# Performance work log

Measured on AMD Instinct MI355X. Metric: run time of the kernel, lower is better.

Reference implementation:

```python
import jax, jax.numpy as jnp
import numpy as np

B = 4096
FEATURES = 4608 + 4608 + 8 + 1  # 9225
LSTM = 512
R = FEATURES / LSTM
D1 = int(FEATURES / R ** (1.0 / 3.0))
D2 = int(FEATURES / R ** (2.0 / 3.0))
ACTION_SHAPES = (64, 64, 64, 64, 64, 64, 64, 64)


def setup_inputs() -> dict:
    key = jax.random.key(0)
    ks = jax.random.split(key, 32)
    s = 0.02
    inp = {
        "actualCanvasFeatures": jax.random.normal(ks[0], (B, 4608), jnp.float32),
        "objectiveCanvasFeatures": jax.random.normal(ks[1], (B, 4608), jnp.float32),
        "last_action": jax.random.uniform(ks[2], (B, 8), jnp.float32),
        "episode_percentage": 0,
        # encoder MLP
        "W1": jax.random.normal(ks[3], (FEATURES, D1), jnp.float32) * s,
        "b1": jnp.zeros((D1,), jnp.float32),
        "W2": jax.random.normal(ks[4], (D1, D2), jnp.float32) * s,
        "b2": jnp.zeros((D2,), jnp.float32),
        "W3": jax.random.normal(ks[5], (D2, LSTM), jnp.float32) * s,
        "b3": jnp.zeros((LSTM,), jnp.float32),
        # LSTM (torch gate order i,f,g,o)
        "Wih": jax.random.normal(ks[6], (4 * LSTM, LSTM), jnp.float32) * s,
        "Whh": jax.random.normal(ks[7], (4 * LSTM, LSTM), jnp.float32) * s,
        "bih": jnp.zeros((4 * LSTM,), jnp.float32),
        "bhh": jnp.zeros((4 * LSTM,), jnp.float32),
        "h0": jnp.zeros((B, LSTM), jnp.float32),
        "c0": jnp.zeros((B, LSTM), jnp.float32),
        # decoder
        "dW1": jax.random.normal(ks[8], (LSTM, LSTM // 2), jnp.float32) * s,
        "db1": jnp.zeros((LSTM // 2,), jnp.float32),
        "headWs": tuple(jax.random.normal(ks[9 + i], (LSTM // 2, a), jnp.float32) * s
                        for i, a in enumerate(ACTION_SHAPES)),
        "headbs": tuple(jnp.zeros((a,), jnp.float32) for a in ACTION_SHAPES),
        "dWo": jax.random.normal(ks[20], (LSTM + 1, LSTM), jnp.float32) * s,
        "dbo": jnp.zeros((LSTM,), jnp.float32),
    }
    return inp


def reference(actualCanvasFeatures, objectiveCanvasFeatures, last_action,
              episode_percentage, W1, b1, W2, b2, W3, b3, Wih, Whh, bih, bhh,
              h0, c0, dW1, db1, headWs, headbs, dWo, dbo):
    b = actualCanvasFeatures.shape[0]
    ep = jnp.full((b, 1), episode_percentage, dtype=jnp.float32)
    feats = jnp.concatenate(
        [actualCanvasFeatures, objectiveCanvasFeatures, last_action, ep], axis=1)
    # encoder MLP (dropout is eval-mode identity)
    x = jax.nn.relu(feats @ W1 + b1)
    x = jax.nn.relu(x @ W2 + b2)
    x = jax.nn.relu(x @ W3 + b3)
    # single-step LSTM cell, torch gate order i,f,g,o
    gates = x @ Wih.T + bih + h0 @ Whh.T + bhh
    i, f, g, o = jnp.split(gates, 4, axis=1)
    c = jax.nn.sigmoid(f) * c0 + jax.nn.sigmoid(i) * jnp.tanh(g)
    z = jax.nn.sigmoid(o) * jnp.tanh(c)  # seed
    key = jax.random.key(42)
    actions = []
    log_probabilities = jnp.zeros((b,), jnp.float32)
    entropy = jnp.float32(0.0)
    for Wk, bk in zip(headWs, headbs):
        z1 = jax.nn.relu(z @ dW1 + db1)
        logits = z1 @ Wk + bk
        logp = jax.nn.log_softmax(logits, axis=1)
        probs = jnp.exp(logp)
        key, sk = jax.random.split(key)
        act = jax.random.categorical(sk, logits, axis=1)  # [b] int
        actions.append(act.astype(jnp.float32))
        entropy = entropy + jnp.sum(-jnp.sum(probs * logp, axis=1))
        log_probabilities = log_probabilities + jnp.take_along_axis(
            logp, act[:, None], axis=1)[:, 0]
        z = jax.nn.relu(
            jnp.concatenate([z, act.astype(jnp.float32)[:, None]], axis=1) @ dWo + dbo)
    action = jnp.stack(actions, axis=1)  # [b, n_sub_actions]
    return action, entropy, log_probabilities
```

## Files before the change

kernel.cpp:

```cpp
#include <hip/hip_runtime.h>
#include <cstdint>
#include <cstring>

typedef _Float16 f16;
typedef _Float16 f16x8 __attribute__((ext_vector_type(8)));
typedef float f32x4 __attribute__((ext_vector_type(4)));

static constexpr int kPartitionable = 1;

struct Ptr8 { const float* p[8]; };

__device__ __host__ __forceinline__ int swz(int r, int k) {
  return k ^ ((r & 7) << 3);
}

__device__ __forceinline__ void gload16(const void* g, void* l) {
  __builtin_amdgcn_global_load_lds(
      (const __attribute__((address_space(1))) unsigned int*)g,
      (__attribute__((address_space(3))) unsigned int*)l, 16, 0, 0);
}

__host__ __device__ inline void tf2x32(uint32_t k0, uint32_t k1,
                                       uint32_t x0, uint32_t x1,
                                       uint32_t& o0, uint32_t& o1) {
  uint32_t ks[3] = {k0, k1, k0 ^ k1 ^ 0x1BD11BDAu};
  uint32_t v0 = x0 + ks[0], v1 = x1 + ks[1];
  const int r0[4] = {13, 15, 26, 6};
  const int r1[4] = {17, 29, 16, 24};
  for (int g = 0; g < 5; ++g) {
    const int* rr = (g & 1) ? r1 : r0;
    for (int j = 0; j < 4; ++j) {
      v0 += v1;
      v1 = (v1 << rr[j]) | (v1 >> (32 - rr[j]));
      v1 ^= v0;
    }
    v0 += ks[(g + 1) % 3];
    v1 += ks[(g + 2) % 3] + (uint32_t)(g + 1);
  }
  o0 = v0; o1 = v1;
}

template <int BM, int BN>
__global__ __launch_bounds__(256, 2) void gemm_split(
    const f16* __restrict__ Ah, const f16* __restrict__ Al, int lda,
    const f16* __restrict__ Bh, const f16* __restrict__ Bl, int ldb,
    int K,
    const float* __restrict__ bias1, const float* __restrict__ bias2,
    int nReal, int relu, int writeF32,
    float* __restrict__ outF, f16* __restrict__ outH, f16* __restrict__ outL,
    int ldo) {
  constexpr int BK = 64;
  constexpr int TM = BM / 32;
  constexpr int TN = BN / 32;
  static_assert(BM == BN, "square tiles only");
  __shared__ f16 sAh[BM * BK];
  __shared__ f16 sAl[BM * BK];
  __shared__ f16 sBh[BN * BK];
  __shared__ f16 sBl[BN * BK];

  const int tid = threadIdx.x;
  const int wave = tid >> 6;
  const int lane = tid & 63;
  const int wm = wave & 1, wn = wave >> 1;
  const int m0 = blockIdx.x * BM;
  const int n0 = blockIdx.y * BN;

  f32x4 acc[TM][TN];
  const f32x4 zero = {0.f, 0.f, 0.f, 0.f};
#pragma unroll
  for (int i = 0; i < TM; ++i)
#pragma unroll
    for (int j = 0; j < TN; ++j) acc[i][j] = zero;

  const f16* src;
  f16* dst;
  int ld, base;
  if (wave == 0)      { src = Ah; dst = sAh; ld = lda; base = m0; }
  else if (wave == 1) { src = Al; dst = sAl; ld = lda; base = m0; }
  else if (wave == 2) { src = Bh; dst = sBh; ld = ldb; base = n0; }
  else                { src = Bl; dst = sBl; ld = ldb; base = n0; }
  constexpr int NITER = BM / 8;
  const f16* gbase = src + (size_t)(base + (lane >> 3)) * ld + (lane & 7) * 8;

  const int fr = lane & 15;
  const int q8 = (lane >> 4) * 8;
  const int sw = (fr & 7) << 3;

  for (int k0 = 0; k0 < K; k0 += BK) {
    __syncthreads();
#pragma unroll
    for (int j = 0; j < NITER; ++j)
      gload16(gbase + (size_t)(j * 8) * ld + k0, dst + j * 512);
    __syncthreads();
#pragma unroll
    for (int kk = 0; kk < BK; kk += 32) {
      const int kf = (kk + q8) ^ sw;
      f16x8 aH[TM], aL[TM], bH[TN], bL[TN];
#pragma unroll
      for (int i = 0; i < TM; ++i) {
        int off = (wm * (BM / 2) + i * 16 + fr) * BK + kf;
        aH[i] = *(const f16x8*)&sAh[off];
        aL[i] = *(const f16x8*)&sAl[off];
      }
#pragma unroll
      for (int j = 0; j < TN; ++j) {
        int off = (wn * (BN / 2) + j * 16 + fr) * BK + kf;
        bH[j] = *(const f16x8*)&sBh[off];
        bL[j] = *(const f16x8*)&sBl[off];
      }
#pragma unroll
      for (int i = 0; i < TM; ++i)
#pragma unroll
        for (int j = 0; j < TN; ++j) {
          acc[i][j] = __builtin_amdgcn_mfma_f32_16x16x32_f16(aH[i], bH[j], acc[i][j], 0, 0, 0);
          acc[i][j] = __builtin_amdgcn_mfma_f32_16x16x32_f16(aH[i], bL[j], acc[i][j], 0, 0, 0);
          acc[i][j] = __builtin_amdgcn_mfma_f32_16x16x32_f16(aL[i], bH[j], acc[i][j], 0, 0, 0);
        }
    }
  }
  const int rq = lane >> 4, cl = lane & 15;
#pragma unroll
  for (int i = 0; i < TM; ++i)
#pragma unroll
    for (int j = 0; j < TN; ++j)
#pragma unroll
      for (int r = 0; r < 4; ++r) {
        int row = m0 + wm * (BM / 2) + i * 16 + rq * 4 + r;
        int col = n0 + wn * (BN / 2) + j * 16 + cl;
        float v = acc[i][j][r];
        if (col < nReal) {
          if (bias1) v += bias1[col];
          if (bias2) v += bias2[col];
          if (relu) v = fmaxf(v, 0.f);
        } else {
          v = 0.f;
        }
        if (writeF32) {
          outF[(size_t)row * ldo + col] = v;
        } else {
          size_t o = (size_t)row * ldo + swz(row, col);
          f16 h = (f16)v;
          outH[o] = h;
          outL[o] = (f16)(v - (float)h);
        }
      }
}

__global__ void conv_feats(const float* __restrict__ A, const float* __restrict__ O,
                           const float* __restrict__ LA, const int* __restrict__ EP,
                           f16* __restrict__ H, f16* __restrict__ L) {
  uint32_t idx = blockIdx.x * 256u + threadIdx.x;
  const uint32_t total = 4096u * 9280u;
  if (idx >= total) return;
  uint32_t b = idx / 9280u, c = idx - b * 9280u;
  float v;
  if (c < 4608u) v = A[(size_t)b * 4608 + c];
  else if (c < 9216u) v = O[(size_t)b * 4608 + (c - 4608u)];
  else if (c < 9224u) v = LA[(size_t)b * 8 + (c - 9216u)];
  else if (c == 9224u) v = (float)EP[0];
  else v = 0.f;
  size_t o = (size_t)b * 9280 + swz((int)b, (int)c);
  f16 h = (f16)v;
  H[o] = h;
  L[o] = (f16)(v - (float)h);
}

__global__ void convT_kernel(const float* __restrict__ W, int Kreal, int Nreal,
                             f16* __restrict__ BtH, f16* __restrict__ BtL, int Kpad) {
  __shared__ float tile[32][33];
  int k0 = blockIdx.x * 32, n0 = blockIdx.y * 32;
  int tx = threadIdx.x, ty = threadIdx.y;
  for (int r = 0; r < 32; r += 8) {
    int k = k0 + ty + r, n = n0 + tx;
    float v = (k < Kreal && n < Nreal) ? W[(size_t)k * Nreal + n] : 0.f;
    tile[ty + r][tx] = v;
  }
  __syncthreads();
  for (int r = 0; r < 32; r += 8) {
    int n = n0 + ty + r, k = k0 + tx;
    float v = tile[tx][ty + r];
    size_t o = (size_t)n * Kpad + swz(n, k);
    f16 h = (f16)v;
    BtH[o] = h;
    BtL[o] = (f16)(v - (float)h);
  }
}

__global__ void convT_heads(Ptr8 ws, f16* __restrict__ BtH, f16* __restrict__ BtL) {
  __shared__ float tile[32][33];
  int h = blockIdx.z;
  const float* W = ws.p[h];
  int k0 = blockIdx.x * 32, n0 = blockIdx.y * 32;
  int tx = threadIdx.x, ty = threadIdx.y;
  for (int r = 0; r < 32; r += 8) {
    int k = k0 + ty + r, n = n0 + tx;
    float v = (k < 256 && n < 64) ? W[(size_t)k * 64 + n] : 0.f;
    tile[ty + r][tx] = v;
  }
  __syncthreads();
  size_t base = (size_t)h * 64 * 256;
  for (int r = 0; r < 32; r += 8) {
    int n = n0 + ty + r, k = k0 + tx;
    float v = tile[tx][ty + r];
    size_t o = base + (size_t)n * 256 + swz(n, k);
    f16 hh = (f16)v;
    BtH[o] = hh;
    BtL[o] = (f16)(v - (float)hh);
  }
}

__global__ void conv_lstmB(const float* __restrict__ Wih, const float* __restrict__ Whh,
                           f16* __restrict__ H, f16* __restrict__ L) {
  uint32_t idx = blockIdx.x * 256u + threadIdx.x;
  uint32_t n = idx >> 10, k = idx & 1023u;
  float v = (k < 512u) ? Wih[(size_t)n * 512 + k] : Whh[(size_t)n * 512 + (k - 512u)];
  size_t o = (size_t)n * 1024 + swz((int)n, (int)k);
  f16 h = (f16)v;
  H[o] = h;
  L[o] = (f16)(v - (float)h);
}

__global__ void conv_h0(const float* __restrict__ h0, f16* __restrict__ H, f16* __restrict__ L) {
  uint32_t idx = blockIdx.x * 256u + threadIdx.x;
  uint32_t b = idx >> 9, j = idx & 511u;
  float v = h0[idx];
  size_t o = (size_t)b * 1024 + swz((int)b, (int)(512 + j));
  f16 h = (f16)v;
  H[o] = h;
  L[o] = (f16)(v - (float)h);
}

__global__ void lstm_pointwise(const float* __restrict__ gates, const float* __restrict__ c0,
                               f16* __restrict__ zH, f16* __restrict__ zL) {
  uint32_t idx = blockIdx.x * 256u + threadIdx.x;
  uint32_t b = idx >> 9, n = idx & 511u;
  const float* g = gates + (size_t)b * 2048;
  float gi = g[n], gf = g[512 + n], gg = g[1024 + n], go = g[1536 + n];
  float si = 1.f / (1.f + expf(-gi));
  float sf = 1.f / (1.f + expf(-gf));
  float so = 1.f / (1.f + expf(-go));
  float c = sf * c0[idx] + si * tanhf(gg);
  float z = so * tanhf(c);
  size_t o = (size_t)b * 576 + swz((int)b, (int)n);
  f16 h = (f16)z;
  zH[o] = h;
  zL[o] = (f16)(z - (float)h);
}

__global__ void init_ws(f16* zAH, f16* zAL, f16* zBH, f16* zBL,
                        float* wsLogp, float* wsEnt) {
  uint32_t idx = blockIdx.x * 256u + threadIdx.x;
  if (idx < 4096u * 63u) {
    uint32_t b = idx / 63u, c = 513u + idx - b * 63u;
    size_t o = (size_t)b * 576 + swz((int)b, (int)c);
    zAH[o] = (f16)0.f; zAL[o] = (f16)0.f; zBH[o] = (f16)0.f; zBL[o] = (f16)0.f;
  }
  if (idx < 4096u) wsLogp[idx] = 0.f;
  if (idx == 0) *wsEnt = 0.f;
}

__device__ inline double shfl_xor_dbl(double v, int m) {
  union { double d; int i[2]; } u;
  u.d = v;
  u.i[0] = __shfl_xor(u.i[0], m);
  u.i[1] = __shfl_xor(u.i[1], m);
  return u.d;
}

__global__ void sample_head(const float* __restrict__ logits,
                            uint32_t sk0, uint32_t sk1, int head, int partitionable,
                            float* __restrict__ outAct,
                            f16* __restrict__ zH, f16* __restrict__ zL,
                            float* __restrict__ wsLogp, float* __restrict__ wsEnt) {
  int wave = threadIdx.x >> 6, lane = threadIdx.x & 63;
  int b = blockIdx.x * 4 + wave;
  float l = logits[(size_t)b * 64 + lane];

  uint32_t i = (uint32_t)b * 64u + (uint32_t)lane;
  uint32_t bits;
  if (partitionable) {
    uint32_t o0, o1;
    tf2x32(sk0, sk1, 0u, i, o0, o1);
    bits = o0 ^ o1;
  } else {
    const uint32_t H = 131072u;
    uint32_t c0, c1, o0, o1;
    int pick;
    if (i < H) { c0 = i; c1 = i + H; pick = 0; }
    else       { c0 = i - H; c1 = i; pick = 1; }
    tf2x32(sk0, sk1, c0, c1, o0, o1);
    bits = pick ? o1 : o0;
  }
  uint32_t ub = (bits >> 9) | 0x3f800000u;
  float u;
  __builtin_memcpy(&u, &ub, 4);
  u -= 1.0f;
  if (u == 0.0f) u = 1.17549435e-38f;
  double gum = -log(-log((double)u));
  double s = (double)l + gum;

  int bi = lane;
  double bv = s;
#pragma unroll
  for (int off = 1; off < 64; off <<= 1) {
    double ov = shfl_xor_dbl(bv, off);
    int oi = __shfl_xor(bi, off);
    if (ov > bv || (ov == bv && oi < bi)) { bv = ov; bi = oi; }
  }
  int act = bi;

  float m = l;
#pragma unroll
  for (int off = 1; off < 64; off <<= 1) m = fmaxf(m, __shfl_xor(m, off));
  float e = expf(l - m);
  float S = e, D = e * l;
#pragma unroll
  for (int off = 1; off < 64; off <<= 1) {
    S += __shfl_xor(S, off);
    D += __shfl_xor(D, off);
  }
  float M = m + logf(S);
  float Hrow = M - D / S;
  float l_act = __shfl(l, act);

  if (lane == 0) {
    outAct[(size_t)b * 8 + head] = (float)act;
    wsLogp[b] += (l_act - M);
    size_t zo = (size_t)b * 576 + swz(b, 512);
    zH[zo] = (f16)act;
    zL[zo] = (f16)0.f;
  }
  __shared__ float hs[4];
  if (lane == 0) hs[wave] = Hrow;
  __syncthreads();
  if (threadIdx.x == 0) atomicAdd(wsEnt, hs[0] + hs[1] + hs[2] + hs[3]);
}

__global__ void finalize_out(const float* __restrict__ wsEnt, const float* __restrict__ wsLogp,
                             float* __restrict__ out) {
  uint32_t idx = blockIdx.x * 256u + threadIdx.x;
  if (idx == 0) out[32768] = *wsEnt;
  if (idx < 4096u) out[32769 + idx] = wsLogp[idx];
}

extern "C" void kernel_launch(void* const* d_in, const int* in_sizes, int n_in,
                              void* d_out, int out_size, void* d_ws, size_t ws_size,
                              hipStream_t stream) {
  (void)in_sizes; (void)out_size; (void)ws_size;
  const float* actual = (const float*)d_in[0];
  const float* object = (const float*)d_in[1];
  const float* lastA = (const float*)d_in[2];
  const int* ep = (const int*)d_in[3];
  const float* W1 = (const float*)d_in[4];
  const float* b1 = (const float*)d_in[5];
  const float* W2 = (const float*)d_in[6];
  const float* b2 = (const float*)d_in[7];
  const float* W3 = (const float*)d_in[8];
  const float* b3 = (const float*)d_in[9];
  const float* Wih = (const float*)d_in[10];
  const float* Whh = (const float*)d_in[11];
  const float* bih = (const float*)d_in[12];
  const float* bhh = (const float*)d_in[13];
  const float* h0 = (const float*)d_in[14];
  const float* c0 = (const float*)d_in[15];
  const float* dW1 = (const float*)d_in[16];
  const float* db1 = (const float*)d_in[17];
  const float* headW[8];
  const float* headb[8];
  const float *dWo, *dbo;
  if (n_in >= 36) {
    for (int h = 0; h < 8; ++h) headW[h] = (const float*)d_in[18 + h];
    for (int h = 0; h < 8; ++h) headb[h] = (const float*)d_in[26 + h];
    dWo = (const float*)d_in[34];
    dbo = (const float*)d_in[35];
  } else {
    const float* hw = (const float*)d_in[18];
    const float* hbp = (const float*)d_in[19];
    for (int h = 0; h < 8; ++h) { headW[h] = hw + (size_t)h * 256 * 64; headb[h] = hbp + (size_t)h * 64; }
    dWo = (const float*)d_in[20];
    dbo = (const float*)d_in[21];
  }

  constexpr int Bq = 4096;
  constexpr int K1 = 9280, N1 = 3584, N1r = 3518;
  constexpr int K2 = 3584, N2 = 1408, N2r = 1342;
  constexpr int K3 = 1408, N3 = 512;
  constexpr int KL = 1024, NL = 2048;
  constexpr int KD1 = 512, ND1 = 256;
  constexpr int KH = 256;
  constexpr int KDO = 576, NDO = 512;

  uint8_t* w = (uint8_t*)d_ws;
  size_t off = 0;
  auto alloc = [&](size_t bytes) -> void* {
    off = (off + 1023) & ~(size_t)1023;
    void* p = w + off;
    off += bytes;
    return p;
  };
  f16* A1h = (f16*)alloc((size_t)Bq * K1 * 2);
  f16* A1l = (f16*)alloc((size_t)Bq * K1 * 2);
  f16* Bt1h = (f16*)alloc((size_t)N1 * K1 * 2);
  f16* Bt1l = (f16*)alloc((size_t)N1 * K1 * 2);
  f16* x1h = (f16*)alloc((size_t)Bq * K2 * 2);
  f16* x1l = (f16*)alloc((size_t)Bq * K2 * 2);
  f16* Bt2h = (f16*)alloc((size_t)N2 * K2 * 2);
  f16* Bt2l = (f16*)alloc((size_t)N2 * K2 * 2);
  size_t poff = 0;
  auto palloc = [&](size_t bytes) -> void* {
    poff = (poff + 1023) & ~(size_t)1023;
    void* p = w + poff;
    poff += bytes;
    return p;
  };
  f16* x2h = (f16*)palloc((size_t)Bq * K3 * 2);
  f16* x2l = (f16*)palloc((size_t)Bq * K3 * 2);
  f16* Bt3h = (f16*)palloc((size_t)N3 * K3 * 2);
  f16* Bt3l = (f16*)palloc((size_t)N3 * K3 * 2);
  f16* ALh = (f16*)palloc((size_t)Bq * KL * 2);
  f16* ALl = (f16*)palloc((size_t)Bq * KL * 2);
  f16* BLh = (f16*)palloc((size_t)NL * KL * 2);
  f16* BLl = (f16*)palloc((size_t)NL * KL * 2);
  float* gates = (float*)palloc((size_t)Bq * NL * 4);
  f16* zAH = (f16*)palloc((size_t)Bq * 576 * 2);
  f16* zAL = (f16*)palloc((size_t)Bq * 576 * 2);
  f16* zBH = (f16*)palloc((size_t)Bq * 576 * 2);
  f16* zBL = (f16*)palloc((size_t)Bq * 576 * 2);
  f16* Btd1h = (f16*)palloc((size_t)ND1 * KD1 * 2);
  f16* Btd1l = (f16*)palloc((size_t)ND1 * KD1 * 2);
  f16* z1h = (f16*)palloc((size_t)Bq * ND1 * 2);
  f16* z1l = (f16*)palloc((size_t)Bq * ND1 * 2);
  f16* Bthh = (f16*)palloc((size_t)8 * 64 * KH * 2);
  f16* Bthl = (f16*)palloc((size_t)8 * 64 * KH * 2);
  float* logitsF = (float*)palloc((size_t)Bq * 64 * 4);
  f16* Btdoh = (f16*)palloc((size_t)NDO * KDO * 2);
  f16* Btdol = (f16*)palloc((size_t)NDO * KDO * 2);
  float* wsLogp = (float*)palloc((size_t)Bq * 4);
  float* wsEnt = (float*)palloc(64);

  uint32_t k0 = 0u, k1 = 42u;
  uint32_t sk[8][2];
  for (int h = 0; h < 8; ++h) {
    if (kPartitionable) {
      uint32_t a0, a1, b0v, b1v;
      tf2x32(k0, k1, 0u, 0u, a0, a1);
      tf2x32(k0, k1, 0u, 1u, b0v, b1v);
      sk[h][0] = b0v; sk[h][1] = b1v;
      k0 = a0; k1 = a1;
    } else {
      uint32_t a0, a1, b0v, b1v;
      tf2x32(k0, k1, 0u, 2u, a0, a1);
      tf2x32(k0, k1, 1u, 3u, b0v, b1v);
      sk[h][0] = a1; sk[h][1] = b1v;
      k0 = a0; k1 = b0v;
    }
  }
  Ptr8 hws;
  for (int h = 0; h < 8; ++h) hws.p[h] = headW[h];

  dim3 blk(256);
  dim3 tblk(32, 8);

  conv_feats<<<(4096u * 9280u + 255) / 256, blk, 0, stream>>>(actual, object, lastA, ep, A1h, A1l);
  convT_kernel<<<dim3(K1 / 32, N1 / 32), tblk, 0, stream>>>(W1, 9225, 3518, Bt1h, Bt1l, K1);
  convT_kernel<<<dim3(K2 / 32, N2 / 32), tblk, 0, stream>>>(W2, 3518, 1342, Bt2h, Bt2l, K2);

  gemm_split<128, 128><<<dim3(Bq / 128, N1 / 128), blk, 0, stream>>>(
      A1h, A1l, K1, Bt1h, Bt1l, K1, K1, b1, nullptr, N1r, 1, 0, nullptr, x1h, x1l, K2);

  init_ws<<<(4096u * 63u + 255) / 256, blk, 0, stream>>>(zAH, zAL, zBH, zBL, wsLogp, wsEnt);
  convT_kernel<<<dim3(K3 / 32, N3 / 32), tblk, 0, stream>>>(W3, 1342, 512, Bt3h, Bt3l, K3);
  conv_lstmB<<<(2048u * 1024u) / 256, blk, 0, stream>>>(Wih, Whh, BLh, BLl);
  conv_h0<<<(4096u * 512u) / 256, blk, 0, stream>>>(h0, ALh, ALl);
  convT_kernel<<<dim3(KD1 / 32, ND1 / 32), tblk, 0, stream>>>(dW1, 512, 256, Btd1h, Btd1l, KD1);
  convT_kernel<<<dim3(KDO / 32, NDO / 32), tblk, 0, stream>>>(dWo, 513, 512, Btdoh, Btdol, KDO);
  convT_heads<<<dim3(KH / 32, 2, 8), tblk, 0, stream>>>(hws, Bthh, Bthl);

  gemm_split<128, 128><<<dim3(Bq / 128, N2 / 128), blk, 0, stream>>>(
      x1h, x1l, K2, Bt2h, Bt2l, K2, K2, b2, nullptr, N2r, 1, 0, nullptr, x2h, x2l, K3);
  gemm_split<128, 128><<<dim3(Bq / 128, N3 / 128), blk, 0, stream>>>(
      x2h, x2l, K3, Bt3h, Bt3l, K3, K3, b3, nullptr, N3, 1, 0, nullptr, ALh, ALl, KL);
  gemm_split<128, 128><<<dim3(Bq / 128, NL / 128), blk, 0, stream>>>(
      ALh, ALl, KL, BLh, BLl, KL, KL, bih, bhh, NL, 0, 1, gates, nullptr, nullptr, NL);
  lstm_pointwise<<<(4096u * 512u) / 256, blk, 0, stream>>>(gates, c0, zAH, zAL);

  for (int h = 0; h < 8; ++h) {
    f16* curH = (h & 1) ? zBH : zAH;
    f16* curL = (h & 1) ? zBL : zAL;
    f16* nxtH = (h & 1) ? zAH : zBH;
    f16* nxtL = (h & 1) ? zAL : zBL;
    gemm_split<64, 64><<<dim3(Bq / 64, ND1 / 64), blk, 0, stream>>>(
        curH, curL, 576, Btd1h, Btd1l, KD1, KD1, db1, nullptr, ND1, 1, 0, nullptr, z1h, z1l, ND1);
    gemm_split<64, 64><<<dim3(Bq / 64, 1), blk, 0, stream>>>(
        z1h, z1l, ND1, Bthh + (size_t)h * 64 * KH, Bthl + (size_t)h * 64 * KH, KH, KH,
        headb[h], nullptr, 64, 0, 1, logitsF, nullptr, nullptr, 64);
    sample_head<<<Bq / 4, blk, 0, stream>>>(logitsF, sk[h][0], sk[h][1], h, kPartitionable,
                                            (float*)d_out, curH, curL, wsLogp, wsEnt);
    gemm_split<64, 64><<<dim3(Bq / 64, NDO / 64), blk, 0, stream>>>(
        curH, curL, 576, Btdoh, Btdol, KDO, KDO, dbo, nullptr, NDO, 1, 0, nullptr, nxtH, nxtL, 576);
  }
  finalize_out<<<(4097 + 255) / 256, blk, 0, stream>>>(wsEnt, wsLogp, (float*)d_out);
}
```

Measured before the change: 1.874 ms.

## Fuse categorical sampling into head GEMM epilogue and vectorize feature conversion

The per-head sampling kernel is folded into the epilogue of the head logits GEMM. Logits stay in shared memory, and each wave handles 16 rows for the Gumbel-max sampling, log-softmax and entropy. This removes eight kernel launches and the logits round trip through global memory. Separately, the feature conversion kernel now handles 8 elements per thread with float4 loads and 16-byte f16x8 stores, replacing scalar accesses. The fused epilogue serializes 16 rows per wave, which may lengthen the tail of a 64-block GEMM.

Measured after the change: 1.943 ms. 1.04x slower.

```diff
diff --git a/kernel.cpp b/kernel.cpp
--- a/kernel.cpp
+++ b/kernel.cpp
@@ -40,7 +40,15 @@
   o0 = v0; o1 = v1;
 }
 
-template <int BM, int BN>
+__device__ inline double shfl_xor_dbl(double v, int m) {
+  union { double d; int i[2]; } u;
+  u.d = v;
+  u.i[0] = __shfl_xor(u.i[0], m);
+  u.i[1] = __shfl_xor(u.i[1], m);
+  return u.d;
+}
+
+template <int BM, int BN, int SAMPLE>
 __global__ __launch_bounds__(256, 2) void gemm_split(
     const f16* __restrict__ Ah, const f16* __restrict__ Al, int lda,
     const f16* __restrict__ Bh, const f16* __restrict__ Bl, int ldb,
@@ -48,7 +56,10 @@
     const float* __restrict__ bias1, const float* __restrict__ bias2,
     int nReal, int relu, int writeF32,
     float* __restrict__ outF, f16* __restrict__ outH, f16* __restrict__ outL,
-    int ldo) {
+    int ldo,
+    uint32_t sk0, uint32_t sk1, int head, int partitionable,
+    float* __restrict__ outAct, f16* __restrict__ zcH, f16* __restrict__ zcL,
+    float* __restrict__ wsLogp, float* __restrict__ wsEnt) {
   constexpr int BK = 64;
   constexpr int TM = BM / 32;
   constexpr int TN = BN / 32;
@@ -119,50 +130,145 @@
     }
   }
   const int rq = lane >> 4, cl = lane & 15;
-#pragma unroll
-  for (int i = 0; i < TM; ++i)
-#pragma unroll
-    for (int j = 0; j < TN; ++j)
-#pragma unroll
-      for (int r = 0; r < 4; ++r) {
-        int row = m0 + wm * (BM / 2) + i * 16 + rq * 4 + r;
-        int col = n0 + wn * (BN / 2) + j * 16 + cl;
-        float v = acc[i][j][r];
-        if (col < nReal) {
-          if (bias1) v += bias1[col];
-          if (bias2) v += bias2[col];
-          if (relu) v = fmaxf(v, 0.f);
-        } else {
-          v = 0.f;
+  if constexpr (SAMPLE) {
+    __shared__ float lgt[64 * 64];
+#pragma unroll
+    for (int i = 0; i < TM; ++i)
+#pragma unroll
+      for (int j = 0; j < TN; ++j)
+#pragma unroll
+        for (int r = 0; r < 4; ++r) {
+          int row = wm * 32 + i * 16 + rq * 4 + r;
+          int col = wn * 32 + j * 16 + cl;
+          lgt[row * 64 + col] = acc[i][j][r] + bias1[col];
         }
-        if (writeF32) {
-          outF[(size_t)row * ldo + col] = v;
-        } else {
-          size_t o = (size_t)row * ldo + swz(row, col);
-          f16 h = (f16)v;
-          outH[o] = h;
-          outL[o] = (f16)(v - (float)h);
+    __syncthreads();
+    float entAcc = 0.f;
+    for (int rr = 0; rr < 16; ++rr) {
+      int row = wave * 16 + rr;
+      int b = m0 + row;
+      float l = lgt[row * 64 + lane];
+      uint32_t i = (uint32_t)b * 64u + (uint32_t)lane;
+      uint32_t bits;
+      if (partitionable) {
+        uint32_t o0, o1;
+        tf2x32(sk0, sk1, 0u, i, o0, o1);
+        bits = o0 ^ o1;
+      } else {
+        const uint32_t Hh = 131072u;
+        uint32_t c0, c1, o0, o1;
+        int pick;
+        if (i < Hh) { c0 = i; c1 = i + Hh; pick = 0; }
+        else        { c0 = i - Hh; c1 = i; pick = 1; }
+        tf2x32(sk0, sk1, c0, c1, o0, o1);
+        bits = pick ? o1 : o0;
+      }
+      uint32_t ub = (bits >> 9) | 0x3f800000u;
+      float u;
+      __builtin_memcpy(&u, &ub, 4);
+      u -= 1.0f;
+      if (u == 0.0f) u = 1.17549435e-38f;
+      double gum = -log(-log((double)u));
+      double s = (double)l + gum;
+      int bi = lane;
+      double bv = s;
+#pragma unroll
+      for (int off = 1; off < 64; off <<= 1) {
+        double ov = shfl_xor_dbl(bv, off);
+        int oi = __shfl_xor(bi, off);
+        if (ov > bv || (ov == bv && oi < bi)) { bv = ov; bi = oi; }
+      }
+      int act = bi;
+      float m = l;
+#pragma unroll
+      for (int off = 1; off < 64; off <<= 1) m = fmaxf(m, __shfl_xor(m, off));
+      float e = expf(l - m);
+      float S = e, D = e * l;
+#pragma unroll
+      for (int off = 1; off < 64; off <<= 1) {
+        S += __shfl_xor(S, off);
+        D += __shfl_xor(D, off);
+      }
+      float M = m + logf(S);
+      entAcc += (M - D / S);
+      float l_act = __shfl(l, act);
+      if (lane == 0) {
+        outAct[(size_t)b * 8 + head] = (float)act;
+        wsLogp[b] += (l_act - M);
+        size_t zo = (size_t)b * 576 + swz(b, 512);
+        zcH[zo] = (f16)act;
+        zcL[zo] = (f16)0.f;
+      }
+    }
+    if (lane == 0) atomicAdd(wsEnt, entAcc);
+  } else {
+#pragma unroll
+    for (int i = 0; i < TM; ++i)
+#pragma unroll
+      for (int j = 0; j < TN; ++j)
+#pragma unroll
+        for (int r = 0; r < 4; ++r) {
+          int row = m0 + wm * (BM / 2) + i * 16 + rq * 4 + r;
+          int col = n0 + wn * (BN / 2) + j * 16 + cl;
+          float v = acc[i][j][r];
+          if (col < nReal) {
+            if (bias1) v += bias1[col];
+            if (bias2) v += bias2[col];
+            if (relu) v = fmaxf(v, 0.f);
+          } else {
+            v = 0.f;
+          }
+          if (writeF32) {
+            outF[(size_t)row * ldo + col] = v;
+          } else {
+            size_t o = (size_t)row * ldo + swz(row, col);
+            f16 h = (f16)v;
+            outH[o] = h;
+            outL[o] = (f16)(v - (float)h);
+          }
         }
-      }
+  }
 }
 
 __global__ void conv_feats(const float* __restrict__ A, const float* __restrict__ O,
                            const float* __restrict__ LA, const int* __restrict__ EP,
                            f16* __restrict__ H, f16* __restrict__ L) {
   uint32_t idx = blockIdx.x * 256u + threadIdx.x;
-  const uint32_t total = 4096u * 9280u;
-  if (idx >= total) return;
-  uint32_t b = idx / 9280u, c = idx - b * 9280u;
-  float v;
-  if (c < 4608u) v = A[(size_t)b * 4608 + c];
-  else if (c < 9216u) v = O[(size_t)b * 4608 + (c - 4608u)];
-  else if (c < 9224u) v = LA[(size_t)b * 8 + (c - 9216u)];
-  else if (c == 9224u) v = (float)EP[0];
-  else v = 0.f;
-  size_t o = (size_t)b * 9280 + swz((int)b, (int)c);
-  f16 h = (f16)v;
-  H[o] = h;
-  L[o] = (f16)(v - (float)h);
+  if (idx >= 4096u * 1160u) return;
+  uint32_t b = idx / 1160u;
+  uint32_t c = (idx - b * 1160u) * 8u;
+  float v[8];
+  if (c < 4608u) {
+    const float4* p = (const float4*)(A + (size_t)b * 4608 + c);
+    float4 x = p[0], y = p[1];
+    v[0] = x.x; v[1] = x.y; v[2] = x.z; v[3] = x.w;
+    v[4] = y.x; v[5] = y.y; v[6] = y.z; v[7] = y.w;
+  } else if (c < 9216u) {
+    const float4* p = (const float4*)(O + (size_t)b * 4608 + (c - 4608u));
+    float4 x = p[0], y = p[1];
+    v[0] = x.x; v[1] = x.y; v[2] = x.z; v[3] = x.w;
+    v[4] = y.x; v[5] = y.y; v[6] = y.z; v[7] = y.w;
+  } else if (c == 9216u) {
+#pragma unroll
+    for (int j = 0; j < 8; ++j) v[j] = LA[(size_t)b * 8 + j];
+  } else if (c == 9224u) {
+    v[0] = (float)EP[0];
+#pragma unroll
+    for (int j = 1; j < 8; ++j) v[j] = 0.f;
+  } else {
+#pragma unroll
+    for (int j = 0; j < 8; ++j) v[j] = 0.f;
+  }
+  size_t o = (size_t)b * 9280 + ((int)c ^ (((int)b & 7) << 3));
+  f16x8 hv, lv;
+#pragma unroll
+  for (int j = 0; j < 8; ++j) {
+    f16 h = (f16)v[j];
+    hv[j] = h;
+    lv[j] = (f16)(v[j] - (float)h);
+  }
+  *(f16x8*)&H[o] = hv;
+  *(f16x8*)&L[o] = lv;
 }
 
 __global__ void convT_kernel(const float* __restrict__ W, int Kreal, int Nreal,
@@ -257,83 +363,6 @@
   }
   if (idx < 4096u) wsLogp[idx] = 0.f;
   if (idx == 0) *wsEnt = 0.f;
-}
-
-__device__ inline double shfl_xor_dbl(double v, int m) {
-  union { double d; int i[2]; } u;
-  u.d = v;
-  u.i[0] = __shfl_xor(u.i[0], m);
-  u.i[1] = __shfl_xor(u.i[1], m);
-  return u.d;
-}
-
-__global__ void sample_head(const float* __restrict__ logits,
-                            uint32_t sk0, uint32_t sk1, int head, int partitionable,
-                            float* __restrict__ outAct,
-                            f16* __restrict__ zH, f16* __restrict__ zL,
-                            float* __restrict__ wsLogp, float* __restrict__ wsEnt) {
-  int wave = threadIdx.x >> 6, lane = threadIdx.x & 63;
-  int b = blockIdx.x * 4 + wave;
-  float l = logits[(size_t)b * 64 + lane];
-
-  uint32_t i = (uint32_t)b * 64u + (uint32_t)lane;
-  uint32_t bits;
-  if (partitionable) {
-    uint32_t o0, o1;
-    tf2x32(sk0, sk1, 0u, i, o0, o1);
-    bits = o0 ^ o1;
-  } else {
-    const uint32_t H = 131072u;
-    uint32_t c0, c1, o0, o1;
-    int pick;
-    if (i < H) { c0 = i; c1 = i + H; pick = 0; }
-    else       { c0 = i - H; c1 = i; pick = 1; }
-    tf2x32(sk0, sk1, c0, c1, o0, o1);
-    bits = pick ? o1 : o0;
-  }
-  uint32_t ub = (bits >> 9) | 0x3f800000u;
-  float u;
-  __builtin_memcpy(&u, &ub, 4);
-  u -= 1.0f;
-  if (u == 0.0f) u = 1.17549435e-38f;
-  double gum = -log(-log((double)u));
-  double s = (double)l + gum;
-
-  int bi = lane;
-  double bv = s;
-#pragma unroll
-  for (int off = 1; off < 64; off <<= 1) {
-    double ov = shfl_xor_dbl(bv, off);
-    int oi = __shfl_xor(bi, off);
-    if (ov > bv || (ov == bv && oi < bi)) { bv = ov; bi = oi; }
-  }
-  int act = bi;
-
-  float m = l;
-#pragma unroll
-  for (int off = 1; off < 64; off <<= 1) m = fmaxf(m, __shfl_xor(m, off));
-  float e = expf(l - m);
-  float S = e, D = e * l;
-#pragma unroll
-  for (int off = 1; off < 64; off <<= 1) {
-    S += __shfl_xor(S, off);
-    D += __shfl_xor(D, off);
-  }
-  float M = m + logf(S);
-  float Hrow = M - D / S;
-  float l_act = __shfl(l, act);
-
-  if (lane == 0) {
-    outAct[(size_t)b * 8 + head] = (float)act;
-    wsLogp[b] += (l_act - M);
-    size_t zo = (size_t)b * 576 + swz(b, 512);
-    zH[zo] = (f16)act;
-    zL[zo] = (f16)0.f;
-  }
-  __shared__ float hs[4];
-  if (lane == 0) hs[wave] = Hrow;
-  __syncthreads();
-  if (threadIdx.x == 0) atomicAdd(wsEnt, hs[0] + hs[1] + hs[2] + hs[3]);
 }
 
 __global__ void finalize_out(const float* __restrict__ wsEnt, const float* __restrict__ wsLogp,
@@ -432,7 +461,6 @@
   f16* z1l = (f16*)palloc((size_t)Bq * ND1 * 2);
   f16* Bthh = (f16*)palloc((size_t)8 * 64 * KH * 2);
   f16* Bthl = (f16*)palloc((size_t)8 * 64 * KH * 2);
-  float* logitsF = (float*)palloc((size_t)Bq * 64 * 4);
   f16* Btdoh = (f16*)palloc((size_t)NDO * KDO * 2);
   f16* Btdol = (f16*)palloc((size_t)NDO * KDO * 2);
   float* wsLogp = (float*)palloc((size_t)Bq * 4);
@@ -461,12 +489,13 @@
   dim3 blk(256);
   dim3 tblk(32, 8);
 
-  conv_feats<<<(4096u * 9280u + 255) / 256, blk, 0, stream>>>(actual, object, lastA, ep, A1h, A1l);
+  conv_feats<<<(4096u * 1160u + 255) / 256, blk, 0, stream>>>(actual, object, lastA, ep, A1h, A1l);
   convT_kernel<<<dim3(K1 / 32, N1 / 32), tblk, 0, stream>>>(W1, 9225, 3518, Bt1h, Bt1l, K1);
   convT_kernel<<<dim3(K2 / 32, N2 / 32), tblk, 0, stream>>>(W2, 3518, 1342, Bt2h, Bt2l, K2);
 
-  gemm_split<128, 128><<<dim3(Bq / 128, N1 / 128), blk, 0, stream>>>(
-      A1h, A1l, K1, Bt1h, Bt1l, K1, K1, b1, nullptr, N1r, 1, 0, nullptr, x1h, x1l, K2);
+  gemm_split<128, 128, 0><<<dim3(Bq / 128, N1 / 128), blk, 0, stream>>>(
+      A1h, A1l, K1, Bt1h, Bt1l, K1, K1, b1, nullptr, N1r, 1, 0, nullptr, x1h, x1l, K2,
+      0, 0, 0, 0, nullptr, nullptr, nullptr, nullptr, nullptr);
 
   init_ws<<<(4096u * 63u + 255) / 256, blk, 0, stream>>>(zAH, zAL, zBH, zBL, wsLogp, wsEnt);
   convT_kernel<<<dim3(K3 / 32, N3 / 32), tblk, 0, stream>>>(W3, 1342, 512, Bt3h, Bt3l, K3);
@@ -476,12 +505,15 @@
   convT_kernel<<<dim3(KDO / 32, NDO / 32), tblk, 0, stream>>>(dWo, 513, 512, Btdoh, Btdol, KDO);
   convT_heads<<<dim3(KH / 32, 2, 8), tblk, 0, stream>>>(hws, Bthh, Bthl);
 
-  gemm_split<128, 128><<<dim3(Bq / 128, N2 / 128), blk, 0, stream>>>(
-      x1h, x1l, K2, Bt2h, Bt2l, K2, K2, b2, nullptr, N2r, 1, 0, nullptr, x2h, x2l, K3);
-  gemm_split<128, 128><<<dim3(Bq / 128, N3 / 128), blk, 0, stream>>>(
-      x2h, x2l, K3, Bt3h, Bt3l, K3, K3, b3, nullptr, N3, 1, 0, nullptr, ALh, ALl, KL);
-  gemm_split<128, 128><<<dim3(Bq / 128, NL / 128), blk, 0, stream>>>(
-      ALh, ALl, KL, BLh, BLl, KL, KL, bih, bhh, NL, 0, 1, gates, nullptr, nullptr, NL);
+  gemm_split<128, 128, 0><<<dim3(Bq / 128, N2 / 128), blk, 0, stream>>>(
+      x1h, x1l, K2, Bt2h, Bt2l, K2, K2, b2, nullptr, N2r, 1, 0, nullptr, x2h, x2l, K3,
+      0, 0, 0, 0, nullptr, nullptr, nullptr, nullptr, nullptr);
+  gemm_split<128, 128, 0><<<dim3(Bq / 128, N3 / 128), blk, 0, stream>>>(
+      x2h, x2l, K3, Bt3h, Bt3l, K3, K3, b3, nullptr, N3, 1, 0, nullptr, ALh, ALl, KL,
+      0, 0, 0, 0, nullptr, nullptr, nullptr, nullptr, nullptr);
+  gemm_split<128, 128, 0><<<dim3(Bq / 128, NL / 128), blk, 0, stream>>>(
+      ALh, ALl, KL, BLh, BLl, KL, KL, bih, bhh, NL, 0, 1, gates, nullptr, nullptr, NL,
+      0, 0, 0, 0, nullptr, nullptr, nullptr, nullptr, nullptr);
   lstm_pointwise<<<(4096u * 512u) / 256, blk, 0, stream>>>(gates, c0, zAH, zAL);
 
   for (int h = 0; h < 8; ++h) {
@@ -489,15 +521,16 @@
     f16* curL = (h & 1) ? zBL : zAL;
     f16* nxtH = (h & 1) ? zAH : zBH;
     f16* nxtL = (h & 1) ? zAL : zBL;
-    gemm_split<64, 64><<<dim3(Bq / 64, ND1 / 64), blk, 0, stream>>>(
-        curH, curL, 576, Btd1h, Btd1l, KD1, KD1, db1, nullptr, ND1, 1, 0, nullptr, z1h, z1l, ND1);
-    gemm_split<64, 64><<<dim3(Bq / 64, 1), blk, 0, stream>>>(
+    gemm_split<64, 64, 0><<<dim3(Bq / 64, ND1 / 64), blk, 0, stream>>>(
+        curH, curL, 576, Btd1h, Btd1l, KD1, KD1, db1, nullptr, ND1, 1, 0, nullptr, z1h, z1l, ND1,
+        0, 0, 0, 0, nullptr, nullptr, nullptr, nullptr, nullptr);
+    gemm_split<64, 64, 1><<<dim3(Bq / 64, 1), blk, 0, stream>>>(
         z1h, z1l, ND1, Bthh + (size_t)h * 64 * KH, Bthl + (size_t)h * 64 * KH, KH, KH,
-        headb[h], nullptr, 64, 0, 1, logitsF, nullptr, nullptr, 64);
-    sample_head<<<Bq / 4, blk, 0, stream>>>(logitsF, sk[h][0], sk[h][1], h, kPartitionable,
-                                            (float*)d_out, curH, curL, wsLogp, wsEnt);
-    gemm_split<64, 64><<<dim3(Bq / 64, NDO / 64), blk, 0, stream>>>(
-        curH, curL, 576, Btdoh, Btdol, KDO, KDO, dbo, nullptr, NDO, 1, 0, nullptr, nxtH, nxtL, 576);
+        headb[h], nullptr, 64, 0, 0, nullptr, nullptr, nullptr, 64,
+        sk[h][0], sk[h][1], h, kPartitionable, (float*)d_out, curH, curL, wsLogp, wsEnt);
+    gemm_split<64, 64, 0><<<dim3(Bq / 64, NDO / 64), blk, 0, stream>>>(
+        curH, curL, 576, Btdoh, Btdol, KDO, KDO, dbo, nullptr, NDO, 1, 0, nullptr, nxtH, nxtL, 576,
+        0, 0, 0, 0, nullptr, nullptr, nullptr, nullptr, nullptr);
   }
   finalize_out<<<(4097 + 255) / 256, blk, 0, stream>>>(wsEnt, wsLogp, (float*)d_out);
 }
```
